# Optimization experiments

Hardware: AMD Instinct MI355X
Metric: run time of the kernel (lower is better)

Reference implementation:

```python
import jax, jax.numpy as jnp
import numpy as np

B, S, HID = 4, 4096, 2048
H, G = 16, 4
D = HID // H  # head_dim = 128
KV = HID * G // H  # k/v proj out dim = 512


def setup_inputs() -> dict:
    key = jax.random.key(0)
    ks = jax.random.split(key, 9)
    s = lambda fan_in: 1.0 / np.sqrt(fan_in)
    return {
        "hidden_states": jax.random.normal(ks[0], (B, S, HID), jnp.float32),
        "Wq": jax.random.uniform(ks[1], (HID, HID), jnp.float32, -s(HID), s(HID)),
        "bq": jnp.zeros((HID,), jnp.float32),
        "Wk": jax.random.uniform(ks[2], (HID, KV), jnp.float32, -s(HID), s(HID)),
        "bk": jnp.zeros((KV,), jnp.float32),
        "Wv": jax.random.uniform(ks[3], (HID, KV), jnp.float32, -s(HID), s(HID)),
        "bv": jnp.zeros((KV,), jnp.float32),
        "Wo": jax.random.uniform(ks[4], (HID, HID), jnp.float32, -s(HID), s(HID)),
        "bo": jnp.zeros((HID,), jnp.float32),
    }


def reference(hidden_states, Wq, bq, Wk, bk, Wv, bv, Wo, bo):
    # Projections (torch Linear: x @ W^T + b; here W stored as [in, out])
    q = hidden_states @ Wq + bq            # [B,S,HID]
    k = hidden_states @ Wk + bk            # [B,S,KV]
    v = hidden_states @ Wv + bv            # [B,S,KV]
    q = q.reshape(B, S, H, D)
    k = k.reshape(B, S, G, D)
    v = v.reshape(B, S, G, D)
    # Faithful to source: scores over groups at the SAME position, [B,S,H,G]
    scores = jnp.einsum("bshd,bsgd->bshg", q, k) / jnp.sqrt(jnp.float32(D))
    probs = jax.nn.softmax(scores, axis=-1)  # softmax over G
    out = jnp.einsum("bshg,bsgd->bshd", probs, v)  # [B,S,H,D]
    out = out.reshape(B, S, HID)
    return out @ Wo + bo
```

## Files before the change

### kernel.cpp

```cpp
#include <hip/hip_runtime.h>
#include <hip/hip_bf16.h>
#include <stdint.h>

typedef __bf16 bf16_t;
typedef __bf16 bf16x8 __attribute__((ext_vector_type(8)));
typedef __bf16 bf16x4_t __attribute__((ext_vector_type(4)));
typedef float f32x4 __attribute__((ext_vector_type(4)));

#define AS1 __attribute__((address_space(1)))
#define AS3 __attribute__((address_space(3)))

__device__ __forceinline__ void stage16(const void* g, void* l) {
    __builtin_amdgcn_global_load_lds((const AS1 uint32_t*)g, (AS3 uint32_t*)l, 16, 0, 0);
}

template <typename OutT>
__global__ __launch_bounds__(256, 2) void gemm_bt_bias(
    const bf16_t* __restrict__ A, int lda,
    const bf16_t* __restrict__ Bt,
    const float* __restrict__ bias,
    OutT* __restrict__ C, int ldc,
    int M, int N, int K)
{
    __shared__ char smem[16384];
    const int tid  = threadIdx.x;
    const int wave = tid >> 6;
    const int lane = tid & 63;
    const int quad = lane >> 4;
    const int mrow = lane & 15;
    const int warpM = wave >> 1;
    const int warpN = wave & 1;
    const int mBase = blockIdx.y * 128;
    const int nBase = blockIdx.x * 128;

    f32x4 acc[4][4];
    const f32x4 fzero = {0.f, 0.f, 0.f, 0.f};
#pragma unroll
    for (int i = 0; i < 4; ++i)
#pragma unroll
        for (int j = 0; j < 4; ++j) acc[i][j] = fzero;

    const int s0 = tid, s1 = 256 + tid;
    const int am0 = s0 >> 2, aj0 = (s0 & 3) ^ ((am0 >> 1) & 3);
    const int am1 = s1 >> 2, aj1 = (s1 & 3) ^ ((am1 >> 1) & 3);
    const bf16_t* aS0 = A  + (size_t)(mBase + am0) * lda + aj0 * 8;
    const bf16_t* aS1 = A  + (size_t)(mBase + am1) * lda + aj1 * 8;
    const bf16_t* bS0 = Bt + (size_t)(nBase + am0) * K + aj0 * 8;
    const bf16_t* bS1 = Bt + (size_t)(nBase + am1) * K + aj1 * 8;
    char* const aD0 = smem + wave * 1024;
    char* const aD1 = smem + 4096  + wave * 1024;
    char* const bD0 = smem + 8192  + wave * 1024;
    char* const bD1 = smem + 12288 + wave * 1024;

    int aOff[4], bOff[4];
#pragma unroll
    for (int i = 0; i < 4; ++i) {
        int m = warpM * 64 + i * 16 + mrow;
        aOff[i] = (m * 4 + (quad ^ ((m >> 1) & 3))) * 16;
        int n = warpN * 64 + i * 16 + mrow;
        bOff[i] = 8192 + (n * 4 + (quad ^ ((n >> 1) & 3))) * 16;
    }

    for (int kt = 0; kt < K; kt += 32) {
        stage16(aS0 + kt, aD0);
        stage16(aS1 + kt, aD1);
        stage16(bS0 + kt, bD0);
        stage16(bS1 + kt, bD1);
        __syncthreads();
        bf16x8 af[4], bfv[4];
#pragma unroll
        for (int i = 0; i < 4; ++i) af[i]  = *(const bf16x8*)(smem + aOff[i]);
#pragma unroll
        for (int j = 0; j < 4; ++j) bfv[j] = *(const bf16x8*)(smem + bOff[j]);
#pragma unroll
        for (int i = 0; i < 4; ++i)
#pragma unroll
            for (int j = 0; j < 4; ++j)
                acc[i][j] = __builtin_amdgcn_mfma_f32_16x16x32_bf16(af[i], bfv[j], acc[i][j], 0, 0, 0);
        __syncthreads();
    }

#pragma unroll
    for (int j = 0; j < 4; ++j) {
        const int col = nBase + warpN * 64 + j * 16 + mrow;
        const float bv = bias[col];
#pragma unroll
        for (int i = 0; i < 4; ++i) {
            const int row = mBase + warpM * 64 + i * 16 + quad * 4;
#pragma unroll
            for (int r = 0; r < 4; ++r)
                C[(size_t)(row + r) * ldc + col] = (OutT)(acc[i][j][r] + bv);
        }
    }
}

__global__ __launch_bounds__(256) void f32_to_bf16(const float* __restrict__ src,
                                                   bf16_t* __restrict__ dst, int n4) {
    int i = blockIdx.x * 256 + threadIdx.x;
    if (i >= n4) return;
    float4 v = ((const float4*)src)[i];
    bf16x4_t o;
    o.x = (bf16_t)v.x; o.y = (bf16_t)v.y; o.z = (bf16_t)v.z; o.w = (bf16_t)v.w;
    ((bf16x4_t*)dst)[i] = o;
}

__global__ __launch_bounds__(256) void transpose_convert(
    const float* __restrict__ src, bf16_t* __restrict__ dst,
    int rows, int cols)
{
    __shared__ bf16_t t[64][65];
    const int tx = threadIdx.x & 63;
    const int ty = threadIdx.x >> 6;
    const int c0 = blockIdx.x * 64;
    const int r0 = blockIdx.y * 64;
#pragma unroll
    for (int r = ty; r < 64; r += 4)
        t[r][tx] = (bf16_t)src[(size_t)(r0 + r) * cols + c0 + tx];
    __syncthreads();
#pragma unroll
    for (int r = ty; r < 64; r += 4)
        dst[(size_t)(c0 + r) * rows + r0 + tx] = t[tx][r];
}

__global__ void concat_bias(const float* __restrict__ bq, const float* __restrict__ bk,
                            const float* __restrict__ bv, float* __restrict__ o) {
    int i = blockIdx.x * 256 + threadIdx.x;
    if (i >= 3072) return;
    o[i] = (i < 2048) ? bq[i] : (i < 2560 ? bk[i - 2048] : bv[i - 2560]);
}

__global__ __launch_bounds__(256) void gqa_attn(
    const bf16_t* __restrict__ q, int sq,
    const bf16_t* __restrict__ kv, int skv,
    bf16_t* __restrict__ out, int so)
{
    const int token = blockIdx.x;
    const int wave = threadIdx.x >> 6, lane = threadIdx.x & 63;
    const bf16_t* qb  = q  + (size_t)token * sq;
    const bf16_t* kvb = kv + (size_t)token * skv;
    const float scale = 0.08838834764831845f;
    float k0[4], k1[4], v0[4], v1[4];
#pragma unroll
    for (int g = 0; g < 4; ++g) {
        uint32_t ku = *(const uint32_t*)(kvb + g * 128 + lane * 2);
        k0[g] = __uint_as_float(ku << 16);
        k1[g] = __uint_as_float(ku & 0xffff0000u);
        uint32_t vu = *(const uint32_t*)(kvb + 512 + g * 128 + lane * 2);
        v0[g] = __uint_as_float(vu << 16);
        v1[g] = __uint_as_float(vu & 0xffff0000u);
    }
#pragma unroll
    for (int hh = 0; hh < 4; ++hh) {
        const int h = wave * 4 + hh;
        uint32_t qu = *(const uint32_t*)(qb + h * 128 + lane * 2);
        float q0 = __uint_as_float(qu << 16);
        float q1 = __uint_as_float(qu & 0xffff0000u);
        float s[4];
#pragma unroll
        for (int g = 0; g < 4; ++g) s[g] = q0 * k0[g] + q1 * k1[g];
#pragma unroll
        for (int off = 32; off > 0; off >>= 1)
#pragma unroll
            for (int g = 0; g < 4; ++g) s[g] += __shfl_xor(s[g], off);
        float mx = fmaxf(fmaxf(s[0], s[1]), fmaxf(s[2], s[3]));
        float e[4], sum = 0.f;
#pragma unroll
        for (int g = 0; g < 4; ++g) { e[g] = __expf((s[g] - mx) * scale); sum += e[g]; }
        const float rs = 1.0f / sum;
        float o0 = 0.f, o1 = 0.f;
#pragma unroll
        for (int g = 0; g < 4; ++g) { o0 += e[g] * v0[g]; o1 += e[g] * v1[g]; }
        o0 *= rs; o1 *= rs;
        bf16_t* op = out + (size_t)token * so + h * 128 + lane * 2;
        op[0] = (bf16_t)o0;
        op[1] = (bf16_t)o1;
    }
}

__global__ __launch_bounds__(256) void compact_q(const bf16_t* __restrict__ src,
                                                 bf16_t* __restrict__ dst) {
    size_t i = (size_t)blockIdx.x * 256 + threadIdx.x;
    size_t t = i >> 8;
    size_t c = (i & 255) * 8;
    *(uint4*)(dst + t * 2048 + c) = *(const uint4*)(src + t * 3072 + c);
}

extern "C" void kernel_launch(void* const* d_in, const int* in_sizes, int n_in,
                              void* d_out, int out_size, void* d_ws, size_t ws_size,
                              hipStream_t stream) {
    const float* hs = (const float*)d_in[0];
    const float* Wq = (const float*)d_in[1];
    const float* bq = (const float*)d_in[2];
    const float* Wk = (const float*)d_in[3];
    const float* bk = (const float*)d_in[4];
    const float* Wv = (const float*)d_in[5];
    const float* bv = (const float*)d_in[6];
    const float* Wo = (const float*)d_in[7];
    const float* bo = (const float*)d_in[8];
    float* outp = (float*)d_out;
    char* ws = (char*)d_ws;

    bf16_t* Wt     = (bf16_t*)(ws);
    bf16_t* Wot    = (bf16_t*)(ws + 12582912);
    float*  bqkv   = (float*)(ws + 20971520);
    bf16_t* hs_b   = (bf16_t*)(ws + 20983808);
    bf16_t* atto   = (bf16_t*)(ws + 20983808);
    bf16_t* qkv    = (bf16_t*)d_out;

    f32_to_bf16<<<32768, 256, 0, stream>>>(hs, hs_b, 8388608);
    transpose_convert<<<dim3(32, 32), 256, 0, stream>>>(Wq, Wt, 2048, 2048);
    transpose_convert<<<dim3(8, 32), 256, 0, stream>>>(Wk, Wt + (size_t)2048 * 2048, 2048, 512);
    transpose_convert<<<dim3(8, 32), 256, 0, stream>>>(Wv, Wt + (size_t)2560 * 2048, 2048, 512);
    transpose_convert<<<dim3(32, 32), 256, 0, stream>>>(Wo, Wot, 2048, 2048);
    concat_bias<<<12, 256, 0, stream>>>(bq, bk, bv, bqkv);

    gemm_bt_bias<bf16_t><<<dim3(24, 128), 256, 0, stream>>>(
        hs_b, 2048, Wt, bqkv, qkv, 3072, 16384, 3072, 2048);
    gqa_attn<<<16384, 256, 0, stream>>>(qkv, 3072, qkv + 2048, 3072, qkv, 3072);
    compact_q<<<16384, 256, 0, stream>>>(qkv, atto);
    gemm_bt_bias<float><<<dim3(16, 128), 256, 0, stream>>>(
        atto, 2048, Wot, bo, outp, 2048, 16384, 2048, 2048);
}
```

Measured before the change: 753.2 us.

## Replace GEMM with 256x256 double-buffered pipelined kernel and drop Q compaction

Replaces the 128x128 single-stage GEMM with a 256x256-tile, 512-thread kernel. It uses 128KB of LDS, double-buffers global-to-LDS loads across phased barriers with s_setprio around the MFMA blocks, and adds a grid swizzle for L2 locality. The attention kernel now writes its output directly into a compact buffer, so the compact_q copy kernel is gone. The aim is to hide load latency and raise data reuse per tile. In exchange it adds register pressure from 32 accumulators per thread and a large LDS footprint that limits occupancy.

```diff
diff --git a/kernel.cpp b/kernel.cpp
--- a/kernel.cpp
+++ b/kernel.cpp
@@ -10,88 +10,126 @@
 #define AS1 __attribute__((address_space(1)))
 #define AS3 __attribute__((address_space(3)))
 
-__device__ __forceinline__ void stage16(const void* g, void* l) {
+__device__ __forceinline__ void stage16(const bf16_t* g, char* l) {
     __builtin_amdgcn_global_load_lds((const AS1 uint32_t*)g, (AS3 uint32_t*)l, 16, 0, 0);
 }
 
+#define BAR()   __builtin_amdgcn_s_barrier()
+#define LGKM0() asm volatile("s_waitcnt lgkmcnt(0)" ::: "memory")
+#define VMC(N)  asm volatile("s_waitcnt vmcnt(" #N ")" ::: "memory")
+#define PRIO(p) __builtin_amdgcn_s_setprio(p)
+
 template <typename OutT>
-__global__ __launch_bounds__(256, 2) void gemm_bt_bias(
+__global__ __launch_bounds__(512, 2) void gemm256(
     const bf16_t* __restrict__ A, int lda,
-    const bf16_t* __restrict__ Bt,
+    const bf16_t* __restrict__ Bt, int ldb,
     const float* __restrict__ bias,
     OutT* __restrict__ C, int ldc,
-    int M, int N, int K)
+    int K, int nTilesN)
 {
-    __shared__ char smem[16384];
+    __shared__ char smem[131072];
     const int tid  = threadIdx.x;
     const int wave = tid >> 6;
     const int lane = tid & 63;
+    const int wm = wave >> 2;
+    const int wn = wave & 3;
+
+    const int bid = blockIdx.x;
+    const int swz = (bid & 7) * ((int)gridDim.x >> 3) + (bid >> 3);
+    const int m0 = (swz / nTilesN) << 8;
+    const int n0 = (swz % nTilesN) << 8;
+
+    const int srow = lane >> 2;
+    const int scol = ((lane & 3) * 8) ^ ((lane & 32) >> 1);
+    const bf16_t* aS0 = A  + (size_t)(m0 + wave * 32 + srow) * lda + scol;
+    const bf16_t* aS1 = aS0 + (size_t)16 * lda;
+    const bf16_t* bS0 = Bt + (size_t)(n0 + wave * 32 + srow) * ldb + scol;
+    const bf16_t* bS1 = bS0 + (size_t)16 * ldb;
+
+#define STAGE_A(b,kk,kb) do { \
+    stage16(aS0 + (kb) + (kk)*32, smem + (b)*65536 + (kk)*16384 + wave*2048); \
+    stage16(aS1 + (kb) + (kk)*32, smem + (b)*65536 + (kk)*16384 + wave*2048 + 1024); } while(0)
+#define STAGE_B(b,kk,kb) do { \
+    stage16(bS0 + (kb) + (kk)*32, smem + (b)*65536 + 32768 + (kk)*16384 + wave*2048); \
+    stage16(bS1 + (kb) + (kk)*32, smem + (b)*65536 + 32768 + (kk)*16384 + wave*2048 + 1024); } while(0)
+
+    const int rdLane = (lane & 15) * 64 + (((lane >> 4) * 16) ^ ((lane & 8) << 2));
+    const char* aRdB = smem + rdLane + wm * 8192;
+    const char* bRdB = smem + 32768 + rdLane + wn * 4096;
+
+    f32x4 acc[8][4];
+#pragma unroll
+    for (int i = 0; i < 8; ++i)
+#pragma unroll
+        for (int j = 0; j < 4; ++j) acc[i][j] = (f32x4){0.f, 0.f, 0.f, 0.f};
+    bf16x8 a[8], bf0, bf1;
+
+#define READ_A(b,kk) { _Pragma("unroll") \
+    for (int mi = 0; mi < 8; ++mi) \
+        a[mi] = *(const bf16x8*)(aRdB + (b)*65536 + (kk)*16384 + mi*1024); }
+#define READ_B(b,kk,nh) { \
+    bf0 = *(const bf16x8*)(bRdB + (b)*65536 + (kk)*16384 + (nh)*2048); \
+    bf1 = *(const bf16x8*)(bRdB + (b)*65536 + (kk)*16384 + (nh)*2048 + 1024); }
+#define MFMA_H(nh) { _Pragma("unroll") \
+    for (int mi = 0; mi < 8; ++mi) { \
+        acc[mi][(nh)*2]   = __builtin_amdgcn_mfma_f32_16x16x32_bf16(a[mi], bf0, acc[mi][(nh)*2],   0, 0, 0); \
+        acc[mi][(nh)*2+1] = __builtin_amdgcn_mfma_f32_16x16x32_bf16(a[mi], bf1, acc[mi][(nh)*2+1], 0, 0, 0); } }
+#define PHASE(RDS, STG, MF, WAIT) do { \
+    RDS; STG; BAR(); LGKM0(); PRIO(1); MF; PRIO(0); WAIT; BAR(); } while(0)
+
+    STAGE_A(0, 0, 0);  STAGE_B(0, 0, 0);  STAGE_A(0, 1, 0);  STAGE_B(0, 1, 0);
+    STAGE_A(1, 0, 64); STAGE_B(1, 0, 64); STAGE_A(1, 1, 64);
+    VMC(6);
+    BAR();
+
+    const int NI = K >> 7;
+    for (int it = 0; it < NI - 1; ++it) {
+        const int kB  = (it << 7) + 64;
+        const int kN0 = (it << 7) + 128;
+        const int kN1 = (it << 7) + 192;
+        PHASE(READ_A(0,0); READ_B(0,0,0), STAGE_B(1,1,kB),  MFMA_H(0), );
+        PHASE(READ_B(0,0,1),              STAGE_A(0,0,kN0), MFMA_H(1), );
+        PHASE(READ_A(0,1); READ_B(0,1,0), STAGE_B(0,0,kN0), MFMA_H(0), );
+        PHASE(READ_B(0,1,1),              STAGE_A(0,1,kN0), MFMA_H(1), VMC(6));
+        PHASE(READ_A(1,0); READ_B(1,0,0), STAGE_B(0,1,kN0), MFMA_H(0), );
+        PHASE(READ_B(1,0,1),              STAGE_A(1,0,kN1), MFMA_H(1), );
+        PHASE(READ_A(1,1); READ_B(1,1,0), STAGE_B(1,0,kN1), MFMA_H(0), );
+        PHASE(READ_B(1,1,1),              STAGE_A(1,1,kN1), MFMA_H(1), VMC(6));
+    }
+    {
+        const int kB = ((NI - 1) << 7) + 64;
+        PHASE(READ_A(0,0); READ_B(0,0,0), STAGE_B(1,1,kB), MFMA_H(0), );
+        PHASE(READ_B(0,0,1),             ,                 MFMA_H(1), );
+        PHASE(READ_A(0,1); READ_B(0,1,0),,                 MFMA_H(0), );
+        PHASE(READ_B(0,1,1),             ,                 MFMA_H(1), VMC(0));
+        PHASE(READ_A(1,0); READ_B(1,0,0),,                 MFMA_H(0), );
+        PHASE(READ_B(1,0,1),             ,                 MFMA_H(1), );
+        PHASE(READ_A(1,1); READ_B(1,1,0),,                 MFMA_H(0), );
+        READ_B(1,1,1); BAR(); LGKM0(); PRIO(1); MFMA_H(1); PRIO(0);
+    }
+
+    const int mrow = lane & 15;
     const int quad = lane >> 4;
-    const int mrow = lane & 15;
-    const int warpM = wave >> 1;
-    const int warpN = wave & 1;
-    const int mBase = blockIdx.y * 128;
-    const int nBase = blockIdx.x * 128;
-
-    f32x4 acc[4][4];
-    const f32x4 fzero = {0.f, 0.f, 0.f, 0.f};
-#pragma unroll
-    for (int i = 0; i < 4; ++i)
-#pragma unroll
-        for (int j = 0; j < 4; ++j) acc[i][j] = fzero;
-
-    const int s0 = tid, s1 = 256 + tid;
-    const int am0 = s0 >> 2, aj0 = (s0 & 3) ^ ((am0 >> 1) & 3);
-    const int am1 = s1 >> 2, aj1 = (s1 & 3) ^ ((am1 >> 1) & 3);
-    const bf16_t* aS0 = A  + (size_t)(mBase + am0) * lda + aj0 * 8;
-    const bf16_t* aS1 = A  + (size_t)(mBase + am1) * lda + aj1 * 8;
-    const bf16_t* bS0 = Bt + (size_t)(nBase + am0) * K + aj0 * 8;
-    const bf16_t* bS1 = Bt + (size_t)(nBase + am1) * K + aj1 * 8;
-    char* const aD0 = smem + wave * 1024;
-    char* const aD1 = smem + 4096  + wave * 1024;
-    char* const bD0 = smem + 8192  + wave * 1024;
-    char* const bD1 = smem + 12288 + wave * 1024;
-
-    int aOff[4], bOff[4];
-#pragma unroll
-    for (int i = 0; i < 4; ++i) {
-        int m = warpM * 64 + i * 16 + mrow;
-        aOff[i] = (m * 4 + (quad ^ ((m >> 1) & 3))) * 16;
-        int n = warpN * 64 + i * 16 + mrow;
-        bOff[i] = 8192 + (n * 4 + (quad ^ ((n >> 1) & 3))) * 16;
-    }
-
-    for (int kt = 0; kt < K; kt += 32) {
-        stage16(aS0 + kt, aD0);
-        stage16(aS1 + kt, aD1);
-        stage16(bS0 + kt, bD0);
-        stage16(bS1 + kt, bD1);
-        __syncthreads();
-        bf16x8 af[4], bfv[4];
-#pragma unroll
-        for (int i = 0; i < 4; ++i) af[i]  = *(const bf16x8*)(smem + aOff[i]);
-#pragma unroll
-        for (int j = 0; j < 4; ++j) bfv[j] = *(const bf16x8*)(smem + bOff[j]);
-#pragma unroll
-        for (int i = 0; i < 4; ++i)
-#pragma unroll
-            for (int j = 0; j < 4; ++j)
-                acc[i][j] = __builtin_amdgcn_mfma_f32_16x16x32_bf16(af[i], bfv[j], acc[i][j], 0, 0, 0);
-        __syncthreads();
-    }
-
-#pragma unroll
-    for (int j = 0; j < 4; ++j) {
-        const int col = nBase + warpN * 64 + j * 16 + mrow;
+    const int cb = n0 + wn * 64 + mrow;
+    const int rb = m0 + wm * 128 + quad * 4;
+#pragma unroll
+    for (int ni = 0; ni < 4; ++ni) {
+        const int col = cb + ni * 16;
         const float bv = bias[col];
 #pragma unroll
-        for (int i = 0; i < 4; ++i) {
-            const int row = mBase + warpM * 64 + i * 16 + quad * 4;
+        for (int mi = 0; mi < 8; ++mi) {
+            const int row = rb + mi * 16;
 #pragma unroll
             for (int r = 0; r < 4; ++r)
-                C[(size_t)(row + r) * ldc + col] = (OutT)(acc[i][j][r] + bv);
+                C[(size_t)(row + r) * ldc + col] = (OutT)(acc[mi][ni][r] + bv);
         }
     }
+#undef STAGE_A
+#undef STAGE_B
+#undef READ_A
+#undef READ_B
+#undef MFMA_H
+#undef PHASE
 }
 
 __global__ __launch_bounds__(256) void f32_to_bf16(const float* __restrict__ src,
@@ -175,14 +213,6 @@
         op[0] = (bf16_t)o0;
         op[1] = (bf16_t)o1;
     }
-}
-
-__global__ __launch_bounds__(256) void compact_q(const bf16_t* __restrict__ src,
-                                                 bf16_t* __restrict__ dst) {
-    size_t i = (size_t)blockIdx.x * 256 + threadIdx.x;
-    size_t t = i >> 8;
-    size_t c = (i & 255) * 8;
-    *(uint4*)(dst + t * 2048 + c) = *(const uint4*)(src + t * 3072 + c);
 }
 
 extern "C" void kernel_launch(void* const* d_in, const int* in_sizes, int n_in,
@@ -214,10 +244,7 @@
     transpose_convert<<<dim3(32, 32), 256, 0, stream>>>(Wo, Wot, 2048, 2048);
     concat_bias<<<12, 256, 0, stream>>>(bq, bk, bv, bqkv);
 
-    gemm_bt_bias<bf16_t><<<dim3(24, 128), 256, 0, stream>>>(
-        hs_b, 2048, Wt, bqkv, qkv, 3072, 16384, 3072, 2048);
-    gqa_attn<<<16384, 256, 0, stream>>>(qkv, 3072, qkv + 2048, 3072, qkv, 3072);
-    compact_q<<<16384, 256, 0, stream>>>(qkv, atto);
-    gemm_bt_bias<float><<<dim3(16, 128), 256, 0, stream>>>(
-        atto, 2048, Wot, bo, outp, 2048, 16384, 2048, 2048);
-}
+    gemm256<bf16_t><<<768, 512, 0, stream>>>(hs_b, 2048, Wt, 2048, bqkv, qkv, 3072, 2048, 12);
+    gqa_attn<<<16384, 256, 0, stream>>>(qkv, 3072, qkv + 2048, 3072, atto, 2048);
+    gemm256<float><<<512, 512, 0, stream>>>(atto, 2048, Wot, 2048, bo, outp, 2048, 2048, 8);
+}
```

Result: faster. 679.9 us (-9.7%).
